# Optimization experiments

Measured on AMD Instinct MI355X. Metric: run time of the kernel, lower is better.

## Reference

```python
import jax, jax.numpy as jnp
import numpy as np

N = 100_000      # nodes
E = 1_600_000    # edges (avg degree 16)
IN, H, OUT = 960, 192, 3
NB = 6           # block_num


def setup_inputs() -> dict:
    key = jax.random.key(0)
    ks = jax.random.split(key, 14)
    s = 0.05  # weight init scale
    x = jax.random.normal(ks[0], (N, IN), jnp.float32)
    src = jax.random.randint(ks[1], (E,), 0, N, jnp.int32)
    dst = jax.random.randint(ks[2], (E,), 0, N, jnp.int32)
    # normalized adjacency values (like D^-1 A entries)
    ew = jax.random.uniform(ks[3], (E,), jnp.float32) / 16.0
    w1 = jax.random.normal(ks[4], (IN, H), jnp.float32) * s
    l1 = jax.random.normal(ks[5], (IN, H), jnp.float32) * s
    b1 = jnp.zeros((H,), jnp.float32)
    wb = jax.random.normal(ks[6], (2 * NB, H, H), jnp.float32) * s
    lb = jax.random.normal(ks[7], (2 * NB, H, H), jnp.float32) * s
    bb = jnp.zeros((2 * NB, H), jnp.float32)
    w2 = jax.random.normal(ks[8], (H, OUT), jnp.float32) * s
    l2 = jax.random.normal(ks[9], (H, OUT), jnp.float32) * s
    b2 = jnp.zeros((OUT,), jnp.float32)
    return dict(x=x, src=src, dst=dst, ew=ew, w1=w1, l1=l1, b1=b1,
                wb=wb, lb=lb, bb=bb, w2=w2, l2=l2, b2=b2)


def reference(x, src, dst, ew, w1, l1, b1, wb, lb, bb, w2, l2, b2):
    def gcn(h, w, lw, b):
        # GraphConvolution: spmm(adj, h @ w) + h @ loop_w + b
        sup = h @ w                                   # [N, F_out]
        msg = sup[src] * ew[:, None]                  # gather + weight  [E, F_out]
        agg = jax.ops.segment_sum(msg, dst, num_segments=N)
        return agg + h @ lw + b

    h = gcn(x, w1, l1, b1)                            # conv1: in_dim -> hidden
    for i in range(NB):                               # GResBlocks
        a = gcn(h, wb[2 * i], lb[2 * i], bb[2 * i])
        a = gcn(a, wb[2 * i + 1], lb[2 * i + 1], bb[2 * i + 1])
        h = (h + a) * 0.5                             # residual scaling
    x_cat = h
    x_out = gcn(x_cat, w2, l2, b2)                    # conv2: hidden -> out_dim
    return (x_out, x_cat)
```

## Files before the change

kernel.cpp:

```cpp
#include <hip/hip_runtime.h>

typedef __attribute__((ext_vector_type(8))) short short8;
typedef __attribute__((ext_vector_type(4))) float f32x4;
typedef __attribute__((ext_vector_type(4))) int int4v;
typedef __attribute__((ext_vector_type(2))) unsigned int u32x2;

__device__ __forceinline__ float bf2f(unsigned short u) {
  return __uint_as_float(((unsigned)u) << 16);
}
__device__ __forceinline__ unsigned short f2bf(float f) {
  unsigned u = __float_as_uint(f);
  return (unsigned short)((u + 0x7FFFu + ((u >> 16) & 1u)) >> 16);
}

#define GLB_CAST(p) ((const __attribute__((address_space(1))) void*)(p))
#define LDS_CAST(p) ((__attribute__((address_space(3))) void*)(p))

__global__ void count_kernel(const int* __restrict__ dst, int* __restrict__ cnt, int E) {
  int e = blockIdx.x * blockDim.x + threadIdx.x;
  if (e < E) atomicAdd(&cnt[dst[e] + 1], 1);
}

__global__ __launch_bounds__(256) void scan_bsum_kernel(const int* __restrict__ cnt,
                                                        int* __restrict__ bsum, int n) {
  __shared__ int buf[256];
  int tid = threadIdx.x;
  int j0 = blockIdx.x * 1024 + tid * 4;
  int s = 0;
#pragma unroll
  for (int k = 0; k < 4; k++) {
    int j = j0 + k;
    if (j < n) s += cnt[j];
  }
  buf[tid] = s;
  __syncthreads();
  for (int off = 128; off > 0; off >>= 1) {
    if (tid < off) buf[tid] += buf[tid + off];
    __syncthreads();
  }
  if (tid == 0) bsum[blockIdx.x] = buf[0];
}

__global__ __launch_bounds__(256) void scan_small_kernel(const int* __restrict__ bsum,
                                                         int* __restrict__ boff, int nb) {
  __shared__ int buf[2][256];
  int tid = threadIdx.x;
  int C = (nb + 255) >> 8;
  int start = tid * C;
  int end = start + C; if (end > nb) end = nb;
  int s = 0;
  for (int j = start; j < end; j++) s += bsum[j];
  buf[0][tid] = s;
  __syncthreads();
  int pin = 0;
  for (int off = 1; off < 256; off <<= 1) {
    int v = buf[pin][tid];
    if (tid >= off) v += buf[pin][tid - off];
    buf[pin ^ 1][tid] = v;
    pin ^= 1;
    __syncthreads();
  }
  int run = (tid == 0) ? 0 : buf[pin][tid - 1];
  for (int j = start; j < end; j++) {
    boff[j] = run;
    run += bsum[j];
  }
}

__global__ __launch_bounds__(256) void scan_final_kernel(const int* __restrict__ cnt,
                                                         const int* __restrict__ boff,
                                                         int* __restrict__ rowptr,
                                                         int* __restrict__ cur,
                                                         int n, int nrows) {
  __shared__ int buf[2][256];
  int tid = threadIdx.x;
  int j0 = blockIdx.x * 1024 + tid * 4;
  int v[4];
  int s = 0;
#pragma unroll
  for (int k = 0; k < 4; k++) {
    int j = j0 + k;
    v[k] = (j < n) ? cnt[j] : 0;
    s += v[k];
  }
  buf[0][tid] = s;
  __syncthreads();
  int pin = 0;
  for (int off = 1; off < 256; off <<= 1) {
    int t = buf[pin][tid];
    if (tid >= off) t += buf[pin][tid - off];
    buf[pin ^ 1][tid] = t;
    pin ^= 1;
    __syncthreads();
  }
  int run = boff[blockIdx.x] + ((tid == 0) ? 0 : buf[pin][tid - 1]);
#pragma unroll
  for (int k = 0; k < 4; k++) {
    int j = j0 + k;
    if (j < n) {
      run += v[k];
      rowptr[j] = run;
      if (j < nrows) cur[j] = run;
    }
  }
}

__global__ void fill_kernel(const int* __restrict__ src, const int* __restrict__ dst,
                            const float* __restrict__ ew,
                            int* __restrict__ cur, int2* __restrict__ s_edge, int E) {
  int e = blockIdx.x * blockDim.x + threadIdx.x;
  if (e >= E) return;
  int r = dst[e];
  int pos = atomicAdd(&cur[r], 1);
  s_edge[pos] = make_int2(src[e], __float_as_int(ew[e]));
}

__global__ void prep_w_kernel(const float* __restrict__ w1,
                              const float* __restrict__ l1,
                              const float* __restrict__ wb,
                              const float* __restrict__ lb,
                              unsigned short* __restrict__ Wt1,
                              unsigned short* __restrict__ Wtb) {
  int tid = blockIdx.x * blockDim.x + threadIdx.x;
  const int n1 = 384 * 960;
  const int nb = 12 * 384 * 192;
  if (tid < n1) {
    int c = tid / 960, k = tid % 960;
    Wt1[tid] = f2bf((c < 192) ? w1[k * 192 + c] : l1[k * 192 + (c - 192)]);
  } else if (tid < n1 + nb) {
    int u = tid - n1;
    int i = u / (384 * 192);
    int r = u % (384 * 192);
    int c = r / 192, k = r % 192;
    Wtb[u] = f2bf((c < 192) ? wb[(i * 192 + k) * 192 + c]
                            : lb[(i * 192 + k) * 192 + (c - 192)]);
  }
}

__device__ __forceinline__ short8 cvt_f32x8(const float* p) {
  f32x4 a = *reinterpret_cast<const f32x4*>(p);
  f32x4 b = *reinterpret_cast<const f32x4*>(p + 4);
  short8 r;
  r[0] = (short)f2bf(a[0]); r[1] = (short)f2bf(a[1]);
  r[2] = (short)f2bf(a[2]); r[3] = (short)f2bf(a[3]);
  r[4] = (short)f2bf(b[0]); r[5] = (short)f2bf(b[1]);
  r[6] = (short)f2bf(b[2]); r[7] = (short)f2bf(b[3]);
  return r;
}

template <typename T>
__global__ __launch_bounds__(512) void gemm_kernel(const T* __restrict__ A,
                                                   const unsigned short* __restrict__ Wt,
                                                   unsigned short* __restrict__ out,
                                                   int nrows, int K) {
  __shared__ char lds_raw[40960];

  int tid = threadIdx.x;
  int lane = tid & 63;
  int w = tid >> 6;
  int rg = w >> 1, ch = w & 1;
  int row0blk = blockIdx.x * 256;
  int row0 = row0blk + rg * 64;
  int l15 = lane & 15, lq = lane >> 4;

  f32x4 acc[12][4];
#pragma unroll
  for (int cf = 0; cf < 12; cf++)
#pragma unroll
    for (int rf = 0; rf < 4; rf++) acc[cf][rf] = (f32x4)(0.0f);

  int tiles = K / 32;
  for (int tile = 0; tile < tiles; ++tile) {
    __syncthreads();
#pragma unroll
    for (int it = 0; it < 3; ++it) {
      int slot = it * 512 + tid;
      int q = slot / 384, c = slot - q * 384;
      const unsigned short* g = Wt + (size_t)c * K + tile * 32 + q * 8;
      __builtin_amdgcn_global_load_lds(GLB_CAST(g), LDS_CAST(lds_raw + 16384 + slot * 16), 16, 0, 0);
    }
#pragma unroll
    for (int it = 0; it < 2; ++it) {
      int slot = it * 512 + tid;
      int c = slot >> 8, row = slot & 255;
      int grow = row0blk + row;
      if (grow > nrows - 1) grow = nrows - 1;
      if constexpr (sizeof(T) == 2) {
        const T* g = A + (size_t)grow * K + tile * 32 + c * 8;
        __builtin_amdgcn_global_load_lds(GLB_CAST(g), LDS_CAST(lds_raw + slot * 16), 16, 0, 0);
      } else {
        const float* g = (const float*)A + (size_t)grow * K + tile * 32 + c * 8;
        *reinterpret_cast<short8*>(lds_raw + slot * 16) = cvt_f32x8(g);
      }
    }
    __syncthreads();

    short8 af[4];
#pragma unroll
    for (int rf = 0; rf < 4; rf++)
      af[rf] = *reinterpret_cast<const short8*>(
          lds_raw + lq * 4096 + (rg * 64 + rf * 16 + l15) * 16);
#pragma unroll
    for (int cf = 0; cf < 12; cf++) {
      const short8 bf = *reinterpret_cast<const short8*>(
          lds_raw + 16384 + (lq * 384 + ch * 192 + cf * 16 + l15) * 16);
#pragma unroll
      for (int rf = 0; rf < 4; rf++)
        acc[cf][rf] = __builtin_amdgcn_mfma_f32_16x16x32_bf16(bf, af[rf], acc[cf][rf], 0, 0, 0);
    }
  }

#pragma unroll
  for (int rf = 0; rf < 4; rf++) {
    int row = row0 + rf * 16 + l15;
    if (row >= nrows) continue;
    unsigned short* orow = out + (size_t)row * 384 + ch * 192 + lq * 4;
#pragma unroll
    for (int cf = 0; cf < 12; cf++) {
      u32x2 pv;
      pv[0] = (unsigned)f2bf(acc[cf][rf][0]) | ((unsigned)f2bf(acc[cf][rf][1]) << 16);
      pv[1] = (unsigned)f2bf(acc[cf][rf][2]) | ((unsigned)f2bf(acc[cf][rf][3]) << 16);
      *reinterpret_cast<u32x2*>(orow + cf * 16) = pv;
    }
  }
}

__global__ __launch_bounds__(256) void spmm_kernel(const unsigned short* __restrict__ t,
                                                   const int* __restrict__ rowptr,
                                                   const int2* __restrict__ s_edge,
                                                   const float* __restrict__ bias,
                                                   const float* __restrict__ hprev32,
                                                   unsigned short* __restrict__ out16,
                                                   float* __restrict__ out32,
                                                   int n, int mode) {
  int tid = blockIdx.x * blockDim.x + threadIdx.x;
  int node = tid / 24;
  int c = tid % 24;
  if (node >= n) return;

  float acc[8];
#pragma unroll
  for (int j = 0; j < 8; j++) acc[j] = 0.0f;

  int e0 = rowptr[node], e1 = rowptr[node + 1];
  int e = e0;
  for (; e + 4 <= e1; e += 4) {
    int2 ra = s_edge[e];
    int2 rb = s_edge[e + 1];
    int2 rc = s_edge[e + 2];
    int2 rd = s_edge[e + 3];
    float wa = __int_as_float(ra.y), wb = __int_as_float(rb.y);
    float wc = __int_as_float(rc.y), wd = __int_as_float(rd.y);
    short8 va = *reinterpret_cast<const short8*>(&t[(size_t)ra.x * 384 + c * 8]);
    short8 vb = *reinterpret_cast<const short8*>(&t[(size_t)rb.x * 384 + c * 8]);
    short8 vc = *reinterpret_cast<const short8*>(&t[(size_t)rc.x * 384 + c * 8]);
    short8 vd = *reinterpret_cast<const short8*>(&t[(size_t)rd.x * 384 + c * 8]);
#pragma unroll
    for (int j = 0; j < 8; j++) {
      acc[j] += wa * bf2f((unsigned short)va[j]) + wb * bf2f((unsigned short)vb[j]) +
                wc * bf2f((unsigned short)vc[j]) + wd * bf2f((unsigned short)vd[j]);
    }
  }
  for (; e < e1; e++) {
    int2 ra = s_edge[e];
    float wa = __int_as_float(ra.y);
    short8 va = *reinterpret_cast<const short8*>(&t[(size_t)ra.x * 384 + c * 8]);
#pragma unroll
    for (int j = 0; j < 8; j++) acc[j] += wa * bf2f((unsigned short)va[j]);
  }

  short8 hlv = *reinterpret_cast<const short8*>(&t[(size_t)node * 384 + 192 + c * 8]);
  float r[8];
#pragma unroll
  for (int j = 0; j < 8; j++)
    r[j] = acc[j] + bf2f((unsigned short)hlv[j]) + bias[c * 8 + j];

  if (mode == 1) {
#pragma unroll
    for (int j = 0; j < 8; j++)
      r[j] = 0.5f * (hprev32[(size_t)node * 192 + c * 8 + j] + r[j]);
  }

  unsigned short o16[8];
#pragma unroll
  for (int j = 0; j < 8; j++) o16[j] = f2bf(r[j]);
  *reinterpret_cast<int4v*>(&out16[(size_t)node * 192 + c * 8]) =
      *reinterpret_cast<const int4v*>(o16);

  if (out32) {
    f32x4 lo, hi;
    lo[0] = r[0]; lo[1] = r[1]; lo[2] = r[2]; lo[3] = r[3];
    hi[0] = r[4]; hi[1] = r[5]; hi[2] = r[6]; hi[3] = r[7];
    *reinterpret_cast<f32x4*>(&out32[(size_t)node * 192 + c * 8]) = lo;
    *reinterpret_cast<f32x4*>(&out32[(size_t)node * 192 + c * 8 + 4]) = hi;
  }
}

__global__ __launch_bounds__(256) void conv2a_kernel(const float* __restrict__ h,
                                                     const float* __restrict__ w2,
                                                     const float* __restrict__ l2,
                                                     const float* __restrict__ b2,
                                                     float* __restrict__ sup2,
                                                     float* __restrict__ hl2, int n) {
  int wid = (blockIdx.x * blockDim.x + threadIdx.x) >> 6;
  int lane = threadIdx.x & 63;
  if (wid >= n) return;
  float sa[3] = {0.f, 0.f, 0.f}, sl[3] = {0.f, 0.f, 0.f};
  for (int k = lane; k < 192; k += 64) {
    float hv = h[(size_t)wid * 192 + k];
#pragma unroll
    for (int j = 0; j < 3; j++) {
      sa[j] += hv * w2[k * 3 + j];
      sl[j] += hv * l2[k * 3 + j];
    }
  }
#pragma unroll
  for (int j = 0; j < 3; j++) {
    for (int off = 32; off > 0; off >>= 1) {
      sa[j] += __shfl_down(sa[j], off);
      sl[j] += __shfl_down(sl[j], off);
    }
  }
  if (lane == 0) {
#pragma unroll
    for (int j = 0; j < 3; j++) {
      sup2[(size_t)wid * 3 + j] = sa[j];
      hl2[(size_t)wid * 3 + j] = sl[j] + b2[j];
    }
  }
}

__global__ __launch_bounds__(256) void conv2b_kernel(const int* __restrict__ rowptr,
                                                     const int2* __restrict__ s_edge,
                                                     const float* __restrict__ sup2,
                                                     const float* __restrict__ hl2,
                                                     float* __restrict__ out, int n) {
  int node = blockIdx.x * blockDim.x + threadIdx.x;
  if (node >= n) return;
  float acc[3] = {0.f, 0.f, 0.f};
  int e0 = rowptr[node], e1 = rowptr[node + 1];
  for (int e = e0; e < e1; e++) {
    int2 rec = s_edge[e];
    float wgt = __int_as_float(rec.y);
#pragma unroll
    for (int j = 0; j < 3; j++) acc[j] += wgt * sup2[(size_t)rec.x * 3 + j];
  }
#pragma unroll
  for (int j = 0; j < 3; j++)
    out[(size_t)node * 3 + j] = acc[j] + hl2[(size_t)node * 3 + j];
}

extern "C" void kernel_launch(void* const* d_in, const int* in_sizes, int n_in,
                              void* d_out, int out_size, void* d_ws, size_t ws_size,
                              hipStream_t stream) {
  const float* x  = (const float*)d_in[0];
  const int* src  = (const int*)d_in[1];
  const int* dst  = (const int*)d_in[2];
  const float* ew = (const float*)d_in[3];
  const float* w1 = (const float*)d_in[4];
  const float* l1 = (const float*)d_in[5];
  const float* b1 = (const float*)d_in[6];
  const float* wb = (const float*)d_in[7];
  const float* lb = (const float*)d_in[8];
  const float* bb = (const float*)d_in[9];
  const float* w2 = (const float*)d_in[10];
  const float* l2 = (const float*)d_in[11];
  const float* b2 = (const float*)d_in[12];
  float* out = (float*)d_out;

  const int N = in_sizes[0] / 960;
  const int E = in_sizes[1];

  float* h32 = out + (size_t)N * 3;

  char* p = (char*)d_ws;
  auto alloc = [&](size_t bytes) {
    char* q = p;
    p += (bytes + 255) & ~(size_t)255;
    return q;
  };
  unsigned short* Wt1 = (unsigned short*)alloc((size_t)384 * 960 * 2);
  unsigned short* Wtb = (unsigned short*)alloc((size_t)12 * 384 * 192 * 2);
  unsigned short* t   = (unsigned short*)alloc((size_t)N * 384 * 2);
  unsigned short* h16 = (unsigned short*)alloc((size_t)N * 192 * 2);
  unsigned short* a16 = (unsigned short*)alloc((size_t)N * 192 * 2);
  int* rowptr = (int*)alloc((size_t)(N + 1) * 4);
  int* cur    = (int*)alloc((size_t)N * 4);
  int* cnt    = (int*)alloc((size_t)(N + 1) * 4);
  int* bsum   = (int*)alloc((size_t)1024 * 4);
  int* boff   = (int*)alloc((size_t)1024 * 4);
  int2* s_edge = (int2*)alloc((size_t)E * 8);
  float* sup2 = (float*)alloc((size_t)N * 3 * 4);
  float* hl2  = (float*)alloc((size_t)N * 3 * 4);
  if ((size_t)(p - (char*)d_ws) > ws_size) return;

  const int nScan = N + 1;
  const int nBlk = (nScan + 1023) / 1024;

  hipMemsetAsync(cnt, 0, (size_t)(N + 1) * 4, stream);
  count_kernel<<<(E + 255) / 256, 256, 0, stream>>>(dst, cnt, E);
  scan_bsum_kernel<<<nBlk, 256, 0, stream>>>(cnt, bsum, nScan);
  scan_small_kernel<<<1, 256, 0, stream>>>(bsum, boff, nBlk);
  scan_final_kernel<<<nBlk, 256, 0, stream>>>(cnt, boff, rowptr, cur, nScan, N);
  fill_kernel<<<(E + 255) / 256, 256, 0, stream>>>(src, dst, ew, cur, s_edge, E);
  {
    int total = 384 * 960 + 12 * 384 * 192;
    prep_w_kernel<<<(total + 255) / 256, 256, 0, stream>>>(w1, l1, wb, lb, Wt1, Wtb);
  }

  int gBlocks = (N + 255) / 256;
  int sBlocks = (N * 24 + 255) / 256;

  gemm_kernel<float><<<gBlocks, 512, 0, stream>>>(x, Wt1, t, N, 960);
  spmm_kernel<<<sBlocks, 256, 0, stream>>>(t, rowptr, s_edge, b1,
                                           (const float*)nullptr, h16, h32, N, 0);

  for (int i = 0; i < 12; i += 2) {
    gemm_kernel<unsigned short><<<gBlocks, 512, 0, stream>>>(
        h16, Wtb + (size_t)i * 384 * 192, t, N, 192);
    spmm_kernel<<<sBlocks, 256, 0, stream>>>(t, rowptr, s_edge, bb + (size_t)i * 192,
                                             (const float*)nullptr, a16, (float*)nullptr, N, 0);
    gemm_kernel<unsigned short><<<gBlocks, 512, 0, stream>>>(
        a16, Wtb + (size_t)(i + 1) * 384 * 192, t, N, 192);
    spmm_kernel<<<sBlocks, 256, 0, stream>>>(t, rowptr, s_edge, bb + (size_t)(i + 1) * 192,
                                             h32, h16, h32, N, 1);
  }

  conv2a_kernel<<<(N + 3) / 4, 256, 0, stream>>>(h32, w2, l2, b2, sup2, hl2, N);
  conv2b_kernel<<<(N + 255) / 256, 256, 0, stream>>>(rowptr, s_edge, sup2, hl2, out, N);
}
```

Baseline: 2.569 ms.

## Shrink GEMM tile to 64 rows per block and unroll SpMM gather by eight

After: 3.030 ms. 1.18x slower.

```diff
diff --git a/kernel.cpp b/kernel.cpp
--- a/kernel.cpp
+++ b/kernel.cpp
@@ -137,9 +137,7 @@
   }
 }
 
-__device__ __forceinline__ short8 cvt_f32x8(const float* p) {
-  f32x4 a = *reinterpret_cast<const f32x4*>(p);
-  f32x4 b = *reinterpret_cast<const f32x4*>(p + 4);
+__device__ __forceinline__ short8 cvt_pair(f32x4 a, f32x4 b) {
   short8 r;
   r[0] = (short)f2bf(a[0]); r[1] = (short)f2bf(a[1]);
   r[2] = (short)f2bf(a[2]); r[3] = (short)f2bf(a[3]);
@@ -149,77 +147,64 @@
 }
 
 template <typename T>
-__global__ __launch_bounds__(512) void gemm_kernel(const T* __restrict__ A,
-                                                   const unsigned short* __restrict__ Wt,
-                                                   unsigned short* __restrict__ out,
-                                                   int nrows, int K) {
-  __shared__ char lds_raw[40960];
+__global__ __launch_bounds__(256, 4) void gemm_kernel(const T* __restrict__ A,
+                                                      const unsigned short* __restrict__ Wt,
+                                                      unsigned short* __restrict__ out,
+                                                      int nrows, int K) {
+  __shared__ char lds[28672];
 
   int tid = threadIdx.x;
   int lane = tid & 63;
-  int w = tid >> 6;
-  int rg = w >> 1, ch = w & 1;
-  int row0blk = blockIdx.x * 256;
-  int row0 = row0blk + rg * 64;
+  int rg = tid >> 6;
+  int row0 = blockIdx.x * 64;
   int l15 = lane & 15, lq = lane >> 4;
 
-  f32x4 acc[12][4];
-#pragma unroll
-  for (int cf = 0; cf < 12; cf++)
-#pragma unroll
-    for (int rf = 0; rf < 4; rf++) acc[cf][rf] = (f32x4)(0.0f);
+  int sq = tid >> 6, srow = tid & 63;
+  int sgrow = row0 + srow;
+  if (sgrow > nrows - 1) sgrow = nrows - 1;
+
+  f32x4 acc[24];
+#pragma unroll
+  for (int cf = 0; cf < 24; cf++) acc[cf] = (f32x4)(0.0f);
 
   int tiles = K / 32;
   for (int tile = 0; tile < tiles; ++tile) {
     __syncthreads();
 #pragma unroll
-    for (int it = 0; it < 3; ++it) {
-      int slot = it * 512 + tid;
+    for (int it = 0; it < 6; ++it) {
+      int slot = it * 256 + tid;
       int q = slot / 384, c = slot - q * 384;
       const unsigned short* g = Wt + (size_t)c * K + tile * 32 + q * 8;
-      __builtin_amdgcn_global_load_lds(GLB_CAST(g), LDS_CAST(lds_raw + 16384 + slot * 16), 16, 0, 0);
-    }
-#pragma unroll
-    for (int it = 0; it < 2; ++it) {
-      int slot = it * 512 + tid;
-      int c = slot >> 8, row = slot & 255;
-      int grow = row0blk + row;
-      if (grow > nrows - 1) grow = nrows - 1;
-      if constexpr (sizeof(T) == 2) {
-        const T* g = A + (size_t)grow * K + tile * 32 + c * 8;
-        __builtin_amdgcn_global_load_lds(GLB_CAST(g), LDS_CAST(lds_raw + slot * 16), 16, 0, 0);
-      } else {
-        const float* g = (const float*)A + (size_t)grow * K + tile * 32 + c * 8;
-        *reinterpret_cast<short8*>(lds_raw + slot * 16) = cvt_f32x8(g);
-      }
+      __builtin_amdgcn_global_load_lds(GLB_CAST(g), LDS_CAST(lds + 4096 + slot * 16), 16, 0, 0);
+    }
+    if constexpr (sizeof(T) == 2) {
+      const unsigned short* g = (const unsigned short*)A + (size_t)sgrow * K + tile * 32 + sq * 8;
+      __builtin_amdgcn_global_load_lds(GLB_CAST(g), LDS_CAST(lds + tid * 16), 16, 0, 0);
+    } else {
+      const float* g = (const float*)A + (size_t)sgrow * K + tile * 32 + sq * 8;
+      f32x4 a0 = *reinterpret_cast<const f32x4*>(g);
+      f32x4 a1 = *reinterpret_cast<const f32x4*>(g + 4);
+      *reinterpret_cast<short8*>(lds + tid * 16) = cvt_pair(a0, a1);
     }
     __syncthreads();
 
-    short8 af[4];
-#pragma unroll
-    for (int rf = 0; rf < 4; rf++)
-      af[rf] = *reinterpret_cast<const short8*>(
-          lds_raw + lq * 4096 + (rg * 64 + rf * 16 + l15) * 16);
-#pragma unroll
-    for (int cf = 0; cf < 12; cf++) {
+    short8 af = *reinterpret_cast<const short8*>(lds + (lq * 64 + rg * 16 + l15) * 16);
+#pragma unroll
+    for (int cf = 0; cf < 24; cf++) {
       const short8 bf = *reinterpret_cast<const short8*>(
-          lds_raw + 16384 + (lq * 384 + ch * 192 + cf * 16 + l15) * 16);
-#pragma unroll
-      for (int rf = 0; rf < 4; rf++)
-        acc[cf][rf] = __builtin_amdgcn_mfma_f32_16x16x32_bf16(bf, af[rf], acc[cf][rf], 0, 0, 0);
-    }
-  }
-
-#pragma unroll
-  for (int rf = 0; rf < 4; rf++) {
-    int row = row0 + rf * 16 + l15;
-    if (row >= nrows) continue;
-    unsigned short* orow = out + (size_t)row * 384 + ch * 192 + lq * 4;
-#pragma unroll
-    for (int cf = 0; cf < 12; cf++) {
+          lds + 4096 + (lq * 384 + cf * 16 + l15) * 16);
+      acc[cf] = __builtin_amdgcn_mfma_f32_16x16x32_bf16(bf, af, acc[cf], 0, 0, 0);
+    }
+  }
+
+  int row = row0 + rg * 16 + l15;
+  if (row < nrows) {
+    unsigned short* orow = out + (size_t)row * 384 + lq * 4;
+#pragma unroll
+    for (int cf = 0; cf < 24; cf++) {
       u32x2 pv;
-      pv[0] = (unsigned)f2bf(acc[cf][rf][0]) | ((unsigned)f2bf(acc[cf][rf][1]) << 16);
-      pv[1] = (unsigned)f2bf(acc[cf][rf][2]) | ((unsigned)f2bf(acc[cf][rf][3]) << 16);
+      pv[0] = (unsigned)f2bf(acc[cf][0]) | ((unsigned)f2bf(acc[cf][1]) << 16);
+      pv[1] = (unsigned)f2bf(acc[cf][2]) | ((unsigned)f2bf(acc[cf][3]) << 16);
       *reinterpret_cast<u32x2*>(orow + cf * 16) = pv;
     }
   }
@@ -244,24 +229,32 @@
 
   int e0 = rowptr[node], e1 = rowptr[node + 1];
   int e = e0;
-  for (; e + 4 <= e1; e += 4) {
+  for (; e + 8 <= e1; e += 8) {
+    int2 rec[8];
+#pragma unroll
+    for (int k = 0; k < 8; k++) rec[k] = s_edge[e + k];
+    short8 v[8];
+#pragma unroll
+    for (int k = 0; k < 8; k++)
+      v[k] = *reinterpret_cast<const short8*>(&t[(size_t)rec[k].x * 384 + c * 8]);
+#pragma unroll
+    for (int k = 0; k < 8; k++) {
+      float wgt = __int_as_float(rec[k].y);
+#pragma unroll
+      for (int j = 0; j < 8; j++) acc[j] += wgt * bf2f((unsigned short)v[k][j]);
+    }
+  }
+  for (; e + 2 <= e1; e += 2) {
     int2 ra = s_edge[e];
     int2 rb = s_edge[e + 1];
-    int2 rc = s_edge[e + 2];
-    int2 rd = s_edge[e + 3];
     float wa = __int_as_float(ra.y), wb = __int_as_float(rb.y);
-    float wc = __int_as_float(rc.y), wd = __int_as_float(rd.y);
     short8 va = *reinterpret_cast<const short8*>(&t[(size_t)ra.x * 384 + c * 8]);
     short8 vb = *reinterpret_cast<const short8*>(&t[(size_t)rb.x * 384 + c * 8]);
-    short8 vc = *reinterpret_cast<const short8*>(&t[(size_t)rc.x * 384 + c * 8]);
-    short8 vd = *reinterpret_cast<const short8*>(&t[(size_t)rd.x * 384 + c * 8]);
-#pragma unroll
-    for (int j = 0; j < 8; j++) {
-      acc[j] += wa * bf2f((unsigned short)va[j]) + wb * bf2f((unsigned short)vb[j]) +
-                wc * bf2f((unsigned short)vc[j]) + wd * bf2f((unsigned short)vd[j]);
-    }
-  }
-  for (; e < e1; e++) {
+#pragma unroll
+    for (int j = 0; j < 8; j++)
+      acc[j] += wa * bf2f((unsigned short)va[j]) + wb * bf2f((unsigned short)vb[j]);
+  }
+  if (e < e1) {
     int2 ra = s_edge[e];
     float wa = __int_as_float(ra.y);
     short8 va = *reinterpret_cast<const short8*>(&t[(size_t)ra.x * 384 + c * 8]);
@@ -408,19 +401,19 @@
     prep_w_kernel<<<(total + 255) / 256, 256, 0, stream>>>(w1, l1, wb, lb, Wt1, Wtb);
   }
 
-  int gBlocks = (N + 255) / 256;
+  int gBlocks = (N + 63) / 64;
   int sBlocks = (N * 24 + 255) / 256;
 
-  gemm_kernel<float><<<gBlocks, 512, 0, stream>>>(x, Wt1, t, N, 960);
+  gemm_kernel<float><<<gBlocks, 256, 0, stream>>>(x, Wt1, t, N, 960);
   spmm_kernel<<<sBlocks, 256, 0, stream>>>(t, rowptr, s_edge, b1,
                                            (const float*)nullptr, h16, h32, N, 0);
 
   for (int i = 0; i < 12; i += 2) {
-    gemm_kernel<unsigned short><<<gBlocks, 512, 0, stream>>>(
+    gemm_kernel<unsigned short><<<gBlocks, 256, 0, stream>>>(
         h16, Wtb + (size_t)i * 384 * 192, t, N, 192);
     spmm_kernel<<<sBlocks, 256, 0, stream>>>(t, rowptr, s_edge, bb + (size_t)i * 192,
                                              (const float*)nullptr, a16, (float*)nullptr, N, 0);
-    gemm_kernel<unsigned short><<<gBlocks, 512, 0, stream>>>(
+    gemm_kernel<unsigned short><<<gBlocks, 256, 0, stream>>>(
         a16, Wtb + (size_t)(i + 1) * 384 * 192, t, N, 192);
     spmm_kernel<<<sBlocks, 256, 0, stream>>>(t, rowptr, s_edge, bb + (size_t)(i + 1) * 192,
                                              h32, h16, h32, N, 1);
```
